# Kernel optimization log

Measured on AMD Instinct MI355X. Metric: run time of the kernel, lower is better.

## Reference

```python
import jax, jax.numpy as jnp
import numpy as np

WINDOW = 11
C1 = 0.01 ** 2
C2 = 0.03 ** 2
PAD = WINDOW // 2


def _box_filter(img, kernel):
    # img: [B,1,H,W], kernel: [1,1,w,w]; SAME padding (odd window)
    return jax.lax.conv_general_dilated(
        img, kernel,
        window_strides=(1, 1),
        padding=[(PAD, PAD), (PAD, PAD)],
        dimension_numbers=('NCHW', 'OIHW', 'NCHW'))


def setup_inputs() -> dict:
    key = jax.random.key(0)
    kx, ky = jax.random.split(key)
    B, C, H, W = 64, 1, 512, 512
    x = jax.random.uniform(kx, (B, C, H, W), dtype=jnp.float32)
    y = jax.random.uniform(ky, (B, C, H, W), dtype=jnp.float32)
    kernel = jnp.ones((1, 1, WINDOW, WINDOW), dtype=jnp.float32) / (WINDOW ** 2)
    return {"x": x, "y": y, "kernel": kernel}


def reference(x, y, kernel):
    mu_x = _box_filter(x, kernel)
    mu_y = _box_filter(y, kernel)
    mu_x2 = mu_x * mu_x
    mu_y2 = mu_y * mu_y
    mu_xy = mu_x * mu_y
    sigma_x2 = _box_filter(x * x, kernel) - mu_x2
    sigma_y2 = _box_filter(y * y, kernel) - mu_y2
    sigma_xy = _box_filter(x * y, kernel) - mu_xy
    ssim_map = ((2.0 * mu_xy + C1) * (2.0 * sigma_xy + C2)) / (
        (mu_x2 + mu_y2 + C1) * (sigma_x2 + sigma_y2 + C2))
    return 1.0 - jnp.mean(ssim_map)
```

## Files before the change

kernel.cpp:

```cpp
#include <hip/hip_runtime.h>


#define IMG_H 512
#define IMG_W 512
#define N_IMG 64
#define RAD   5
#define SH    4
#define NBAND 32
#define NBLOCKS (N_IMG * NBAND)

#define C1_SSIM 1.0e-4f
#define C2_SSIM 9.0e-4f

__global__ __launch_bounds__(256) void ssim_fused(const float* __restrict__ x,
                                                  const float* __restrict__ y,
                                                  float* __restrict__ part)
{
    const int tx  = threadIdx.x & 63;
    const int ts  = threadIdx.x >> 6;
    const int img = blockIdx.x >> 5;
    const int bnd = blockIdx.x & (NBAND - 1);
    const int r0  = bnd * (4 * SH) + ts * SH;
    const int c0  = tx * 8;

    const float* __restrict__ xb = x + (size_t)img * (IMG_H * IMG_W) + c0;
    const float* __restrict__ yb = y + (size_t)img * (IMG_H * IMG_W) + c0;

    float Vx[8], Vy[8], Vxx[8], Vyy[8], Vxy[8];
#pragma unroll
    for (int j = 0; j < 8; ++j) { Vx[j] = 0.f; Vy[j] = 0.f; Vxx[j] = 0.f; Vyy[j] = 0.f; Vxy[j] = 0.f; }

    auto accum_add = [&](int ri) {
        const float4* xr = (const float4*)(xb + (size_t)ri * IMG_W);
        const float4* yr = (const float4*)(yb + (size_t)ri * IMG_W);
        float4 x0 = xr[0], x1 = xr[1];
        float4 y0 = yr[0], y1 = yr[1];
        float xs[8] = {x0.x, x0.y, x0.z, x0.w, x1.x, x1.y, x1.z, x1.w};
        float ys[8] = {y0.x, y0.y, y0.z, y0.w, y1.x, y1.y, y1.z, y1.w};
#pragma unroll
        for (int j = 0; j < 8; ++j) {
            Vx[j]  += xs[j];
            Vy[j]  += ys[j];
            Vxx[j] = fmaf(xs[j], xs[j], Vxx[j]);
            Vyy[j] = fmaf(ys[j], ys[j], Vyy[j]);
            Vxy[j] = fmaf(xs[j], ys[j], Vxy[j]);
        }
    };

    auto hsum = [&](const float (&V)[8], float (&S)[8]) {
        float w[18];
#pragma unroll
        for (int k = 0; k < 5; ++k) {
            float l = __shfl_up(V[3 + k], 1, 64);
            w[k] = (tx == 0) ? 0.f : l;
        }
#pragma unroll
        for (int j = 0; j < 8; ++j) w[5 + j] = V[j];
#pragma unroll
        for (int k = 0; k < 5; ++k) {
            float r = __shfl_down(V[k], 1, 64);
            w[13 + k] = (tx == 63) ? 0.f : r;
        }
        float s = 0.f;
#pragma unroll
        for (int t = 0; t < 11; ++t) s += w[t];
        S[0] = s;
#pragma unroll
        for (int j = 1; j < 8; ++j) { s += w[j + 10] - w[j - 1]; S[j] = s; }
    };

#pragma unroll 1
    for (int ri = r0 - RAD; ri < r0 + RAD; ++ri)
        if (ri >= 0 && ri < IMG_H) accum_add(ri);

    const float inv121 = 1.0f / 121.0f;
    float loss = 0.0f;

#pragma unroll 1
    for (int ro = r0; ro < r0 + SH; ++ro) {
        int ra = ro + RAD;
        if (ra < IMG_H) accum_add(ra);

        int  rs      = ro - RAD;
        bool haveSub = (rs >= 0);
        float4 sx0, sx1, sy0, sy1;
        if (haveSub) {
            const float4* xr = (const float4*)(xb + (size_t)rs * IMG_W);
            const float4* yr = (const float4*)(yb + (size_t)rs * IMG_W);
            sx0 = xr[0]; sx1 = xr[1]; sy0 = yr[0]; sy1 = yr[1];
        }

        float Sx[8], Sy[8], Sxx[8], Syy[8], Sxy[8];
        hsum(Vx,  Sx);
        hsum(Vy,  Sy);
        hsum(Vxx, Sxx);
        hsum(Vyy, Syy);
        hsum(Vxy, Sxy);

#pragma unroll
        for (int j = 0; j < 8; ++j) {
            float mx  = Sx[j] * inv121;
            float my  = Sy[j] * inv121;
            float mx2 = mx * mx;
            float my2 = my * my;
            float mxy = mx * my;
            float vx  = Sxx[j] * inv121 - mx2;
            float vy  = Syy[j] * inv121 - my2;
            float vxy = Sxy[j] * inv121 - mxy;
            float num = (2.0f * mxy + C1_SSIM) * (2.0f * vxy + C2_SSIM);
            float den = (mx2 + my2 + C1_SSIM) * (vx + vy + C2_SSIM);
            loss += __fdividef(num, den);
        }

        if (haveSub) {
            float xs[8] = {sx0.x, sx0.y, sx0.z, sx0.w, sx1.x, sx1.y, sx1.z, sx1.w};
            float ys[8] = {sy0.x, sy0.y, sy0.z, sy0.w, sy1.x, sy1.y, sy1.z, sy1.w};
#pragma unroll
            for (int j = 0; j < 8; ++j) {
                Vx[j]  -= xs[j];
                Vy[j]  -= ys[j];
                Vxx[j] = fmaf(-xs[j], xs[j], Vxx[j]);
                Vyy[j] = fmaf(-ys[j], ys[j], Vyy[j]);
                Vxy[j] = fmaf(-xs[j], ys[j], Vxy[j]);
            }
        }
    }

#pragma unroll
    for (int off = 32; off > 0; off >>= 1)
        loss += __shfl_down(loss, off, 64);

    __shared__ float pr[4];
    if (tx == 0) pr[ts] = loss;
    __syncthreads();
    if (threadIdx.x == 0)
        part[blockIdx.x] = (pr[0] + pr[1]) + (pr[2] + pr[3]);
}

__global__ __launch_bounds__(256) void ssim_reduce(const float* __restrict__ part,
                                                   float* __restrict__ out)
{
    const int t  = threadIdx.x;
    const int tx = t & 63;
    float s = 0.f;
#pragma unroll
    for (int k = 0; k < NBLOCKS / 256; ++k)
        s += part[t + k * 256];
#pragma unroll
    for (int off = 32; off > 0; off >>= 1)
        s += __shfl_down(s, off, 64);
    __shared__ float ws[4];
    if (tx == 0) ws[t >> 6] = s;
    __syncthreads();
    if (t == 0) {
        float total = (ws[0] + ws[1]) + (ws[2] + ws[3]);
        out[0] = 1.0f - total * (1.0f / ((float)N_IMG * IMG_H * IMG_W));
    }
}

extern "C" void kernel_launch(void* const* d_in, const int* in_sizes, int n_in,
                              void* d_out, int out_size, void* d_ws, size_t ws_size,
                              hipStream_t stream) {
    const float* x = (const float*)d_in[0];
    const float* y = (const float*)d_in[1];
    float* part = (float*)d_ws;

    ssim_fused<<<NBLOCKS, 256, 0, stream>>>(x, y, part);
    ssim_reduce<<<1, 256, 0, stream>>>(part, (float*)d_out);
}
```

Measured before the change: 190.5 us.

## Prefetch window rows into LDS via async global_load_lds and enlarge row strips

```diff
diff --git a/kernel.cpp b/kernel.cpp
--- a/kernel.cpp
+++ b/kernel.cpp
@@ -1,49 +1,75 @@
 #include <hip/hip_runtime.h>
+#include <stdint.h>
 
 
 #define IMG_H 512
 #define IMG_W 512
 #define N_IMG 64
 #define RAD   5
-#define SH    4
-#define NBAND 32
-#define NBLOCKS (N_IMG * NBAND)
+#define SH    16
+#define NBANDG 8
+#define NBLOCKS (N_IMG * NBANDG)
 
 #define C1_SSIM 1.0e-4f
 #define C2_SSIM 9.0e-4f
+
+#define SLOT_BYTES 4096
+
+typedef __attribute__((address_space(3))) uint32_t lds_u32_t;
+typedef const __attribute__((address_space(1))) uint32_t glb_u32_t;
+
+__device__ __forceinline__ void dma16(void* lds, const void* g) {
+    __builtin_amdgcn_global_load_lds((glb_u32_t*)g, (lds_u32_t*)lds, 16, 0, 0);
+}
 
 __global__ __launch_bounds__(256) void ssim_fused(const float* __restrict__ x,
                                                   const float* __restrict__ y,
                                                   float* __restrict__ part)
 {
+    __shared__ __align__(16) char ring[4][2][SLOT_BYTES];
+
     const int tx  = threadIdx.x & 63;
     const int ts  = threadIdx.x >> 6;
-    const int img = blockIdx.x >> 5;
-    const int bnd = blockIdx.x & (NBAND - 1);
-    const int r0  = bnd * (4 * SH) + ts * SH;
+    const int img = blockIdx.x >> 3;
+    const int bg  = blockIdx.x & (NBANDG - 1);
+    const int r0  = bg * (4 * SH) + ts * SH;
     const int c0  = tx * 8;
 
-    const float* __restrict__ xb = x + (size_t)img * (IMG_H * IMG_W) + c0;
-    const float* __restrict__ yb = y + (size_t)img * (IMG_H * IMG_W) + c0;
+    const float* __restrict__ xi = x + (size_t)img * (IMG_H * IMG_W);
+    const float* __restrict__ yi = y + (size_t)img * (IMG_H * IMG_W);
+
+    auto dma_row = [&](char* s, int ri) -> float {
+        int rc = ri < 0 ? 0 : (ri > IMG_H - 1 ? IMG_H - 1 : ri);
+        float sc = (ri >= 0 && ri < IMG_H) ? 1.0f : 0.0f;
+        const char* xg = (const char*)(xi + (size_t)rc * IMG_W) + tx * 16;
+        const char* yg = (const char*)(yi + (size_t)rc * IMG_W) + tx * 16;
+        dma16(s,        xg);
+        dma16(s + 1024, xg + 1024);
+        dma16(s + 2048, yg);
+        dma16(s + 3072, yg + 1024);
+        return sc;
+    };
 
     float Vx[8], Vy[8], Vxx[8], Vyy[8], Vxy[8];
 #pragma unroll
     for (int j = 0; j < 8; ++j) { Vx[j] = 0.f; Vy[j] = 0.f; Vxx[j] = 0.f; Vyy[j] = 0.f; Vxy[j] = 0.f; }
 
-    auto accum_add = [&](int ri) {
-        const float4* xr = (const float4*)(xb + (size_t)ri * IMG_W);
-        const float4* yr = (const float4*)(yb + (size_t)ri * IMG_W);
+    auto accum_lds = [&](const char* s, float f) {
+        const float4* xr = (const float4*)(s + (size_t)tx * 32);
+        const float4* yr = (const float4*)(s + 2048 + (size_t)tx * 32);
         float4 x0 = xr[0], x1 = xr[1];
         float4 y0 = yr[0], y1 = yr[1];
         float xs[8] = {x0.x, x0.y, x0.z, x0.w, x1.x, x1.y, x1.z, x1.w};
         float ys[8] = {y0.x, y0.y, y0.z, y0.w, y1.x, y1.y, y1.z, y1.w};
 #pragma unroll
         for (int j = 0; j < 8; ++j) {
-            Vx[j]  += xs[j];
-            Vy[j]  += ys[j];
-            Vxx[j] = fmaf(xs[j], xs[j], Vxx[j]);
-            Vyy[j] = fmaf(ys[j], ys[j], Vyy[j]);
-            Vxy[j] = fmaf(xs[j], ys[j], Vxy[j]);
+            float fx = f * xs[j];
+            float fy = f * ys[j];
+            Vx[j] += fx;
+            Vy[j] += fy;
+            Vxx[j] = fmaf(fx, xs[j], Vxx[j]);
+            Vyy[j] = fmaf(fy, ys[j], Vyy[j]);
+            Vxy[j] = fmaf(fx, ys[j], Vxy[j]);
         }
     };
 
@@ -69,24 +95,32 @@
         for (int j = 1; j < 8; ++j) { s += w[j + 10] - w[j - 1]; S[j] = s; }
     };
 
+    char* cur = &ring[ts][0][0];
+    char* nxt = &ring[ts][1][0];
+
+    float scCur = dma_row(cur, r0 - 5);
 #pragma unroll 1
-    for (int ri = r0 - RAD; ri < r0 + RAD; ++ri)
-        if (ri >= 0 && ri < IMG_H) accum_add(ri);
+    for (int i = 0; i < 2 * RAD; ++i) {
+        accum_lds(cur, scCur);
+        float scN = dma_row(nxt, r0 - 4 + i);
+        char* t = cur; cur = nxt; nxt = t;
+        scCur = scN;
+    }
 
     const float inv121 = 1.0f / 121.0f;
     float loss = 0.0f;
 
 #pragma unroll 1
     for (int ro = r0; ro < r0 + SH; ++ro) {
-        int ra = ro + RAD;
-        if (ra < IMG_H) accum_add(ra);
+        accum_lds(cur, scCur);
+        float scN = dma_row(nxt, ro + 6);
 
         int  rs      = ro - RAD;
         bool haveSub = (rs >= 0);
         float4 sx0, sx1, sy0, sy1;
         if (haveSub) {
-            const float4* xr = (const float4*)(xb + (size_t)rs * IMG_W);
-            const float4* yr = (const float4*)(yb + (size_t)rs * IMG_W);
+            const float4* xr = (const float4*)(xi + (size_t)rs * IMG_W + c0);
+            const float4* yr = (const float4*)(yi + (size_t)rs * IMG_W + c0);
             sx0 = xr[0]; sx1 = xr[1]; sy0 = yr[0]; sy1 = yr[1];
         }
 
@@ -124,6 +158,9 @@
                 Vxy[j] = fmaf(-xs[j], ys[j], Vxy[j]);
             }
         }
+
+        char* t = cur; cur = nxt; nxt = t;
+        scCur = scN;
     }
 
 #pragma unroll
@@ -142,10 +179,7 @@
 {
     const int t  = threadIdx.x;
     const int tx = t & 63;
-    float s = 0.f;
-#pragma unroll
-    for (int k = 0; k < NBLOCKS / 256; ++k)
-        s += part[t + k * 256];
+    float s = part[t] + part[t + 256];
 #pragma unroll
     for (int off = 32; off > 0; off >>= 1)
         s += __shfl_down(s, off, 64);
```

Measured after the change: 173.2 us. 9.1% less time.
